# Optimization experiments

Hardware: AMD Instinct MI355X
Metric: run time of the kernel (lower is better)

The kernel has to match this reference:

```python
import jax, jax.numpy as jnp
import numpy as np

ALPHA = 0.9
NEG_SLOPE = 0.01  # nn.LeakyReLU default
PAD = 1           # circular padding

def _conv_circular(t, W, b):
    # circular pad spatial dims, then VALID conv (matches padding_mode='circular')
    tp = jnp.pad(t, ((0, 0), (0, 0), (PAD, PAD), (PAD, PAD)), mode='wrap')
    y = jax.lax.conv_general_dilated(
        tp, W, window_strides=(1, 1), padding='VALID',
        dimension_numbers=('NCHW', 'OIHW', 'NCHW'))
    return y + b[None, :, None, None]

def setup_inputs() -> dict:
    key = jax.random.key(0)
    k1, k2, k3, k4 = jax.random.split(key, 4)
    x = jax.random.normal(k1, (32, 64, 56, 56), dtype=jnp.float32)
    n = jax.random.normal(k2, (32, 64, 56, 56), dtype=jnp.float32)
    fan_in = 64 * 3 * 3
    W = jax.random.normal(k3, (256, 64, 3, 3), dtype=jnp.float32) / np.sqrt(fan_in)
    b = jax.random.normal(k4, (256,), dtype=jnp.float32) * 0.01
    return {"x": x, "n": n, "W": W, "b": b}

def reference(x, n, W, b):
    h1 = _conv_circular(x, W, b)            # [B, N, C, F]
    hn = _conv_circular(n, W, b)            # [B, N, C, F]
    B, N, C, F = h1.shape
    xf = h1.reshape(B, N, C * F)            # tran(x) again == h1
    nf = hn.reshape(B, N, C * F)
    a = jnp.einsum('bnf,bmf->bnm', xf, nf)  # [B, N, M]
    a = jnp.where(a >= 0, a, NEG_SLOPE * a) # LeakyReLU
    attn = jax.nn.softmax(a, axis=1)        # Softmax(dim=1): over rows
    agg = jnp.einsum('bnm,bmf->bnf', attn, xf).reshape(B, N, C, F)
    return (1.0 - ALPHA) * agg + ALPHA * h1
```

## Files before the change

### kernel.cpp

```cpp
#include <hip/hip_runtime.h>
#include <hip/hip_bf16.h>
#include <cstddef>

#define SP 3136
#define CIN 64
#define COUT 256
#define NB 32
#define NEG_SLOPE 0.01f

typedef __attribute__((ext_vector_type(8))) short short8v;
typedef __attribute__((ext_vector_type(4))) float f32x4;

__device__ __forceinline__ float bfr(ushort h) {
    union { uint u; float f; } c; c.u = ((uint)h) << 16; return c.f;
}
__device__ __forceinline__ ushort bf_hi(float v) {
    __hip_bfloat16 h = __float2bfloat16(v);
    return *(ushort*)&h;
}

#define SWZ(row, g) ((((g) ^ ((row) & 7))) * 8)

#define GLOAD_LDS(gp, lp) __builtin_amdgcn_global_load_lds(                    \
    (const __attribute__((address_space(1))) void*)(gp),                       \
    (__attribute__((address_space(3))) void*)(lp), 16, 0, 0)

__global__ __launch_bounds__(256)
void pack_w(const float* __restrict__ W, ushort* __restrict__ wh)
{
    const int id = blockIdx.x * 256 + threadIdx.x;
    const int ci = id & 63, co = (id >> 6) & 255, tap = id >> 14;
    float v = W[(size_t)(co * 64 + ci) * 9 + tap];
    const int ks = ci >> 5, cig = (ci >> 3) & 3, ce = ci & 7;
    const size_t o = (((size_t)(tap * 2 + ks) * 4 + cig) * 256 + co) * 8 + ce;
    wh[o] = bf_hi(v);
}

__global__ __launch_bounds__(256, 2)
void conv_fused(const float* __restrict__ xsrc, const float* __restrict__ nsrc,
                const ushort* __restrict__ Wf_hi,
                const float* __restrict__ bias,
                ushort* __restrict__ h1h, ushort* __restrict__ hnh)
{
    __shared__ __align__(16) ushort Bh[4 * 58 * 64];
    const int tid = threadIdx.x;
    const int w = tid >> 6, l = tid & 63;
    const int bid = blockIdx.x;
    const int xcd = bid & 7, s = bid >> 3;
    const int rp  = s % 28;
    const int img = xcd + 8 * (s / 28);
    const int imgb = img & (NB - 1);
    const int y0 = rp * 2, p0 = rp * 112;
    const int co_w = w * 64;
    const bool isX = (img < NB);

    const float* __restrict__ src = (isX ? xsrc : nsrc) + (size_t)imgb * CIN * SP;
    ushort* __restrict__ dh = (isX ? h1h : hnh) + (size_t)imgb * COUT * SP;

    {
        const int j = tid >> 6, ci = tid & 63;
        const int sy = (y0 + 55 + j) % 56;
        const float* r = src + (size_t)ci * SP + sy * 56;
        const int rowb = (j * 58) << 6;
        ushort first = 0, last = 0;
        #pragma unroll
        for (int q = 0; q < 14; ++q) {
            float4 v = *(const float4*)(r + 4 * q);
            #pragma unroll
            for (int e = 0; e < 4; ++e) {
                const int c = 4 * q + e;
                const float vv = (e == 0) ? v.x : (e == 1) ? v.y : (e == 2) ? v.z : v.w;
                const ushort hv = bf_hi(vv);
                if (c == 0)  first = hv;
                if (c == 55) last  = hv;
                const int x = c + 1;
                Bh[rowb + (x << 6) + ((((ci >> 3) ^ (x & 7))) << 3) + (ci & 7)] = hv;
            }
        }
        Bh[rowb + (0 << 6)  + ((((ci >> 3) ^ 0)) << 3) + (ci & 7)] = last;
        Bh[rowb + (57 << 6) + ((((ci >> 3) ^ 1)) << 3) + (ci & 7)] = first;
    }
    __syncthreads();

    f32x4 acc[4][7];
    {
        const int rr = (l >> 4) * 4;
        #pragma unroll
        for (int m = 0; m < 4; ++m) {
            const int cb = co_w + 16 * m + rr;
            f32x4 bv = { bias[cb], bias[cb + 1], bias[cb + 2], bias[cb + 3] };
            #pragma unroll
            for (int nf = 0; nf < 7; ++nf) acc[m][nf] = bv;
        }
    }

    int b58[7], bx[7];
    #pragma unroll
    for (int nf = 0; nf < 7; ++nf) {
        const int sp = nf * 16 + (l & 15);
        const int ry = (sp >= 56) ? 1 : 0;
        const int xx = sp - ry * 56;
        b58[nf] = ry * 58 + xx;
        bx[nf]  = xx;
    }

    size_t aoff[4];
    #pragma unroll
    for (int m = 0; m < 4; ++m)
        aoff[m] = ((size_t)(l >> 4) * 256 + co_w + 16 * m + (l & 15)) * 8;

    short8v cah[4];
    #pragma unroll
    for (int m = 0; m < 4; ++m)
        cah[m] = *(const short8v*)(Wf_hi + aoff[m]);

    for (int it = 0; it < 18; ++it) {
        const int tap = it >> 1, ks = it & 1;
        const int dy = tap / 3, dx = tap - dy * 3;
        const int toff = dy * 58 + dx;
        const int grp = ks * 4 + (l >> 4);

        short8v nah[4];
        {
            const size_t po = (size_t)(it < 17 ? it + 1 : it) * 8192;
            #pragma unroll
            for (int m = 0; m < 4; ++m)
                nah[m] = *(const short8v*)(Wf_hi + aoff[m] + po);
        }

        #pragma unroll
        for (int nf = 0; nf < 7; ++nf) {
            const int x  = bx[nf] + dx;
            const int bi = ((b58[nf] + toff) << 6) + ((grp ^ (x & 7)) << 3);
            short8v bh = *(const short8v*)&Bh[bi];
            #pragma unroll
            for (int m = 0; m < 4; ++m)
                acc[m][nf] = __builtin_amdgcn_mfma_f32_16x16x32_bf16(cah[m], bh, acc[m][nf], 0, 0, 0);
        }
        #pragma unroll
        for (int m = 0; m < 4; ++m) cah[m] = nah[m];
    }

    const int rr = (l >> 4) * 4, cc = l & 15;
    #pragma unroll
    for (int m = 0; m < 4; ++m) {
        const int cb = co_w + 16 * m + rr;
        #pragma unroll
        for (int nf = 0; nf < 7; ++nf) {
            const int p = p0 + nf * 16 + cc;
            #pragma unroll
            for (int r = 0; r < 4; ++r)
                dh[(size_t)(cb + r) * SP + p] = bf_hi(acc[m][nf][r]);
        }
    }
}

__global__ __launch_bounds__(256, 2)
void gemm_a_mfma(const ushort* __restrict__ h1h, const ushort* __restrict__ hnh,
                 float* __restrict__ attn)
{
    __shared__ __align__(16) ushort Ah[64][64];
    __shared__ __align__(16) ushort Bh[64][64];
    const int tid = threadIdx.x;
    const int w = tid >> 6, l = tid & 63;
    const int wn = w >> 1, wm = w & 1;
    const int bid = blockIdx.x;
    const int xcd = bid & 7, s = bid >> 3;
    const int tile = s % 16;
    const int img  = xcd + 8 * (s / 16);
    const int n0 = (tile & 3) * 64, m0 = (tile >> 2) * 64;

    const ushort* __restrict__ mat0 = h1h + ((size_t)img * COUT + n0) * SP;
    const ushort* __restrict__ mat1 = hnh + ((size_t)img * COUT + m0) * SP;

    f32x4 acc[2][2];
    #pragma unroll
    for (int i = 0; i < 2; ++i)
        #pragma unroll
        for (int j = 0; j < 2; ++j) acc[i][j] = (f32x4){0.f, 0.f, 0.f, 0.f};

    const int lr = l >> 3, gp = l & 7;
    const int glog = gp ^ lr;
    const ushort* gptr[4];
    ushort* lptr[4];
    #pragma unroll
    for (int t = 0; t < 4; ++t) {
        const int u = 4 * w + t, mat = u >> 3, seg = u & 7;
        const ushort* ms = (mat == 0) ? mat0 : mat1;
        ushort* lb = (mat == 0) ? &Ah[0][0] : &Bh[0][0];
        gptr[t] = ms + (size_t)(seg * 8 + lr) * SP + glog * 8;
        lptr[t] = lb + seg * 8 * 64;
    }

    for (int k0 = 0; k0 < SP; k0 += 64) {
        #pragma unroll
        for (int t = 0; t < 4; ++t)
            GLOAD_LDS(gptr[t] + k0, lptr[t]);
        __syncthreads();

        #pragma unroll
        for (int ks = 0; ks < 2; ++ks) {
            const int grp = ks * 4 + (l >> 4);
            short8v ahf[2], bhf[2];
            #pragma unroll
            for (int i = 0; i < 2; ++i) {
                const int ar_ = 32 * wn + 16 * i + (l & 15);
                ahf[i] = *(const short8v*)&Ah[ar_][SWZ(ar_, grp)];
                const int br_ = 32 * wm + 16 * i + (l & 15);
                bhf[i] = *(const short8v*)&Bh[br_][SWZ(br_, grp)];
            }
            #pragma unroll
            for (int i = 0; i < 2; ++i)
                #pragma unroll
                for (int j = 0; j < 2; ++j)
                    acc[i][j] = __builtin_amdgcn_mfma_f32_16x16x32_bf16(ahf[i], bhf[j], acc[i][j], 0, 0, 0);
        }
        __syncthreads();
    }

    const int rr = (l >> 4) * 4, cc = l & 15;
    float* __restrict__ aimg = attn + (size_t)img * COUT * COUT;
    #pragma unroll
    for (int i = 0; i < 2; ++i) {
        const int nb = n0 + 32 * wn + 16 * i + rr;
        #pragma unroll
        for (int j = 0; j < 2; ++j) {
            const int m = m0 + 32 * wm + 16 * j + cc;
            #pragma unroll
            for (int r = 0; r < 4; ++r) {
                float v = acc[i][j][r];
                v = (v >= 0.f) ? v : NEG_SLOPE * v;
                aimg[(size_t)(nb + r) * COUT + m] = v;
            }
        }
    }
}

__global__ __launch_bounds__(64)
void softmax_k(const float* __restrict__ attn, ushort* __restrict__ attnb)
{
    const int b = blockIdx.y;
    const int m = blockIdx.x * 64 + threadIdx.x;
    const float* a = attn + (size_t)b * COUT * COUT;
    ushort* ab = attnb + (size_t)b * COUT * COUT;
    float mx = -1e30f;
    for (int n_ = 0; n_ < COUT; ++n_) mx = fmaxf(mx, a[n_ * COUT + m]);
    float s = 0.f;
    for (int n_ = 0; n_ < COUT; ++n_) s += expf(a[n_ * COUT + m] - mx);
    float inv = 1.f / s;
    for (int n_ = 0; n_ < COUT; ++n_)
        ab[n_ * COUT + m] = bf_hi(expf(a[n_ * COUT + m] - mx) * inv);
}

__global__ __launch_bounds__(256, 4)
void gemm_agg_mfma(const ushort* __restrict__ attnb,
                   const ushort* __restrict__ h1h,
                   float* __restrict__ out)
{
    __shared__ __align__(16) ushort Ah[128][64];
    __shared__ __align__(16) ushort Bh[112][76];
    const int tid = threadIdx.x, w = tid >> 6, l = tid & 63;
    const int bid = blockIdx.x;
    const int xcd = bid & 7, s = bid >> 3;
    const int local = s % 56;
    const int img  = xcd + 8 * (s / 56);
    const int f0 = (local % 28) * 112;
    const int n0 = (local / 28) * 128;

    const ushort* __restrict__ A  = attnb + (size_t)img * COUT * COUT;
    const ushort* __restrict__ Hh = h1h + (size_t)img * COUT * SP;

    f32x4 acc[2][7];
    #pragma unroll
    for (int nf = 0; nf < 2; ++nf)
        #pragma unroll
        for (int mf = 0; mf < 7; ++mf) acc[nf][mf] = (f32x4){0.f, 0.f, 0.f, 0.f};

    const int lr = l >> 3, gp = l & 7;
    const int glog = gp ^ lr;
    const ushort* agp[4];
    ushort* alp[4];
    #pragma unroll
    for (int t = 0; t < 4; ++t) {
        const int seg = 4 * w + t;
        agp[t] = A + (size_t)(n0 + seg * 8 + lr) * COUT + glog * 8;
        alp[t] = &Ah[0][0] + seg * 8 * 64;
    }
    const int bm = tid >> 2, bq = tid & 3, bfo = bq * 28;

    for (int k0 = 0; k0 < COUT; k0 += 64) {
        #pragma unroll
        for (int t = 0; t < 4; ++t)
            GLOAD_LDS(agp[t] + k0, alp[t]);
        {
            const ushort* g = Hh + (size_t)(k0 + bm) * SP + f0 + bfo;
            #pragma unroll
            for (int e = 0; e < 7; ++e) {
                uint2 v = *(const uint2*)(g + 4 * e);
                const ushort* vp = (const ushort*)&v;
                #pragma unroll
                for (int j = 0; j < 4; ++j)
                    Bh[bfo + 4 * e + j][bm] = vp[j];
            }
        }
        __syncthreads();
        #pragma unroll
        for (int ks = 0; ks < 2; ++ks) {
            const int grp = ks * 4 + (l >> 4);
            const int kb = ks * 32 + (l >> 4) * 8;
            short8v ah[2];
            #pragma unroll
            for (int nf = 0; nf < 2; ++nf) {
                const int row = 32 * w + 16 * nf + (l & 15);
                ah[nf] = *(const short8v*)&Ah[row][SWZ(row, grp)];
            }
            #pragma unroll
            for (int mf = 0; mf < 7; ++mf) {
                const int br = mf * 16 + (l & 15);
                short8v bh = *(const short8v*)&Bh[br][kb];
                #pragma unroll
                for (int nf = 0; nf < 2; ++nf)
                    acc[nf][mf] = __builtin_amdgcn_mfma_f32_16x16x32_bf16(ah[nf], bh, acc[nf][mf], 0, 0, 0);
            }
        }
        __syncthreads();
    }

    const int rr = (l >> 4) * 4, cc = l & 15;
    float* __restrict__ orow = out + (size_t)img * COUT * SP;
    #pragma unroll
    for (int nf = 0; nf < 2; ++nf) {
        const int nb = n0 + 32 * w + 16 * nf + rr;
        #pragma unroll
        for (int mf = 0; mf < 7; ++mf) {
            const int f = f0 + 16 * mf + cc;
            #pragma unroll
            for (int r = 0; r < 4; ++r) {
                const int n = nb + r;
                float h = bfr(Hh[(size_t)n * SP + f]);
                orow[(size_t)n * SP + f] = 0.1f * acc[nf][mf][r] + 0.9f * h;
            }
        }
    }
}

extern "C" void kernel_launch(void* const* d_in, const int* in_sizes, int n_in,
                              void* d_out, int out_size, void* d_ws, size_t ws_size,
                              hipStream_t stream)
{
    const float* x    = (const float*)d_in[0];
    const float* nn   = (const float*)d_in[1];
    const float* W    = (const float*)d_in[2];
    const float* bias = (const float*)d_in[3];
    float* out = (float*)d_out;

    ushort* h1b_hi = (ushort*)d_ws;
    char*   zone   = (char*)(h1b_hi + (size_t)NB * COUT * SP);
    ushort* Wf_hi  = (ushort*)zone;
    float*  attn   = (float*)zone;
    ushort* attnb  = (ushort*)(zone + (size_t)NB * COUT * COUT * sizeof(float));
    ushort* hnb_hi = (ushort*)d_out;

    pack_w    <<<576, 256, 0, stream>>>(W, Wf_hi);
    conv_fused<<<1792, 256, 0, stream>>>(x, nn, Wf_hi, bias, h1b_hi, hnb_hi);
    gemm_a_mfma  <<<512, 256, 0, stream>>>(h1b_hi, hnb_hi, attn);
    softmax_k    <<<dim3(4, NB), 64, 0, stream>>>(attn, attnb);
    gemm_agg_mfma<<<1792, 256, 0, stream>>>(attnb, h1b_hi, out);
}
```

Baseline: 197.8 us.

## Load attention GEMM operands directly into registers with prefetch, dropping LDS staging

```diff
diff --git a/kernel.cpp b/kernel.cpp
--- a/kernel.cpp
+++ b/kernel.cpp
@@ -159,8 +159,6 @@
 void gemm_a_mfma(const ushort* __restrict__ h1h, const ushort* __restrict__ hnh,
                  float* __restrict__ attn)
 {
-    __shared__ __align__(16) ushort Ah[64][64];
-    __shared__ __align__(16) ushort Bh[64][64];
     const int tid = threadIdx.x;
     const int w = tid >> 6, l = tid & 63;
     const int wn = w >> 1, wm = w & 1;
@@ -170,8 +168,8 @@
     const int img  = xcd + 8 * (s / 16);
     const int n0 = (tile & 3) * 64, m0 = (tile >> 2) * 64;
 
-    const ushort* __restrict__ mat0 = h1h + ((size_t)img * COUT + n0) * SP;
-    const ushort* __restrict__ mat1 = hnh + ((size_t)img * COUT + m0) * SP;
+    const ushort* __restrict__ A = h1h + ((size_t)img * COUT + n0) * SP;
+    const ushort* __restrict__ B = hnh + ((size_t)img * COUT + m0) * SP;
 
     f32x4 acc[2][2];
     #pragma unroll
@@ -179,50 +177,54 @@
         #pragma unroll
         for (int j = 0; j < 2; ++j) acc[i][j] = (f32x4){0.f, 0.f, 0.f, 0.f};
 
-    const int lr = l >> 3, gp = l & 7;
-    const int glog = gp ^ lr;
-    const ushort* gptr[4];
-    ushort* lptr[4];
-    #pragma unroll
-    for (int t = 0; t < 4; ++t) {
-        const int u = 4 * w + t, mat = u >> 3, seg = u & 7;
-        const ushort* ms = (mat == 0) ? mat0 : mat1;
-        ushort* lb = (mat == 0) ? &Ah[0][0] : &Bh[0][0];
-        gptr[t] = ms + (size_t)(seg * 8 + lr) * SP + glog * 8;
-        lptr[t] = lb + seg * 8 * 64;
-    }
+    const int lr16 = l & 15, hi4 = l >> 4;
+    const ushort* pa[2];
+    const ushort* pb[2];
+    #pragma unroll
+    for (int i = 0; i < 2; ++i) {
+        pa[i] = A + (size_t)(32 * wn + 16 * i + lr16) * SP + hi4 * 8;
+        pb[i] = B + (size_t)(32 * wm + 16 * i + lr16) * SP + hi4 * 8;
+    }
+
+    short8v ca[2][2], cb[2][2];
+    #pragma unroll
+    for (int ks = 0; ks < 2; ++ks)
+        #pragma unroll
+        for (int i = 0; i < 2; ++i) {
+            ca[ks][i] = *(const short8v*)(pa[i] + ks * 32);
+            cb[ks][i] = *(const short8v*)(pb[i] + ks * 32);
+        }
 
     for (int k0 = 0; k0 < SP; k0 += 64) {
-        #pragma unroll
-        for (int t = 0; t < 4; ++t)
-            GLOAD_LDS(gptr[t] + k0, lptr[t]);
-        __syncthreads();
-
-        #pragma unroll
-        for (int ks = 0; ks < 2; ++ks) {
-            const int grp = ks * 4 + (l >> 4);
-            short8v ahf[2], bhf[2];
+        const int kn = (k0 + 64 < SP) ? k0 + 64 : k0;
+        short8v na[2][2], nb[2][2];
+        #pragma unroll
+        for (int ks = 0; ks < 2; ++ks)
             #pragma unroll
             for (int i = 0; i < 2; ++i) {
-                const int ar_ = 32 * wn + 16 * i + (l & 15);
-                ahf[i] = *(const short8v*)&Ah[ar_][SWZ(ar_, grp)];
-                const int br_ = 32 * wm + 16 * i + (l & 15);
-                bhf[i] = *(const short8v*)&Bh[br_][SWZ(br_, grp)];
-            }
+                na[ks][i] = *(const short8v*)(pa[i] + kn + ks * 32);
+                nb[ks][i] = *(const short8v*)(pb[i] + kn + ks * 32);
+            }
+
+        #pragma unroll
+        for (int ks = 0; ks < 2; ++ks)
             #pragma unroll
             for (int i = 0; i < 2; ++i)
                 #pragma unroll
                 for (int j = 0; j < 2; ++j)
-                    acc[i][j] = __builtin_amdgcn_mfma_f32_16x16x32_bf16(ahf[i], bhf[j], acc[i][j], 0, 0, 0);
-        }
-        __syncthreads();
+                    acc[i][j] = __builtin_amdgcn_mfma_f32_16x16x32_bf16(ca[ks][i], cb[ks][j], acc[i][j], 0, 0, 0);
+
+        #pragma unroll
+        for (int ks = 0; ks < 2; ++ks)
+            #pragma unroll
+            for (int i = 0; i < 2; ++i) { ca[ks][i] = na[ks][i]; cb[ks][i] = nb[ks][i]; }
     }
 
     const int rr = (l >> 4) * 4, cc = l & 15;
     float* __restrict__ aimg = attn + (size_t)img * COUT * COUT;
     #pragma unroll
     for (int i = 0; i < 2; ++i) {
-        const int nb = n0 + 32 * wn + 16 * i + rr;
+        const int nb2 = n0 + 32 * wn + 16 * i + rr;
         #pragma unroll
         for (int j = 0; j < 2; ++j) {
             const int m = m0 + 32 * wm + 16 * j + cc;
@@ -230,7 +232,7 @@
             for (int r = 0; r < 4; ++r) {
                 float v = acc[i][j][r];
                 v = (v >= 0.f) ? v : NEG_SLOPE * v;
-                aimg[(size_t)(nb + r) * COUT + m] = v;
+                aimg[(size_t)(nb2 + r) * COUT + m] = v;
             }
         }
     }
```

Measured after the change: 251.5 us. 1.27x slower.
